# Kernel tuning notes

Hardware: AMD Instinct MI355X
Metric: run time of the kernel (lower is better)

Reference implementation:

```python
import jax, jax.numpy as jnp
import numpy as np
import math

HEIGHT = 256
THRESH = int(HEIGHT / (2 * math.sqrt(2)))  # 90, as in Spectral_Discriminator.__init__
EPS = 1e-8


def _radial_bins(h, w):
    # Static (numpy) integer radius of each pixel from the spectrum center.
    y, x = np.indices((h, w))
    cx, cy = (w - 1) / 2.0, (h - 1) / 2.0
    r = np.hypot(x - cx, y - cy)
    r_int = r.astype(np.int64).ravel()           # [h*w]
    nbins = int(r_int.max()) + 1                 # ~ h/sqrt(2) + 1 bins
    return jnp.asarray(r_int), nbins


def get_fft_feature(x):
    # x: [B, 3, H, W] -> azimuthally averaged log power spectrum [B, nbins]
    gray = 0.2989 * x[:, 0] + 0.5870 * x[:, 1] + 0.1140 * x[:, 2]   # [B,H,W]
    f = jnp.fft.fft2(gray)                                           # complex64
    mag = jnp.log(jnp.abs(f) + EPS)                                  # log magnitude
    mag = jnp.fft.fftshift(mag, axes=(-2, -1))                       # center DC
    B, h, w = mag.shape
    r_int, nbins = _radial_bins(h, w)
    flat = mag.reshape(B, -1)                                        # [B, h*w]
    # radial (azimuthal-average) binning: segment mean by integer radius
    sums = jax.vmap(lambda v: jax.ops.segment_sum(v, r_int, num_segments=nbins))(flat)
    counts = jax.ops.segment_sum(jnp.ones((h * w,), jnp.float32), r_int, num_segments=nbins)
    prof = sums / counts                                             # [B, nbins]
    # per-sample min-max normalization (NaN if max==min; masked by caller)
    mn = prof.min(axis=1, keepdims=True)
    mx = prof.max(axis=1, keepdims=True)
    return (prof - mn) / (mx - mn)


def setup_inputs() -> dict:
    key = jax.random.key(0)
    k1, k2 = jax.random.split(key)
    x = jax.random.normal(k1, (128, 3, HEIGHT, HEIGHT), dtype=jnp.float32)
    w = jax.random.normal(k2, (1, THRESH), dtype=jnp.float32) * (1.0 / math.sqrt(THRESH))
    b = jnp.zeros((1,), dtype=jnp.float32)
    return {"x": x, "w": w, "b": b}


def reference(x, w, b):
    feat = get_fft_feature(x)                          # [B, nbins]
    feat = jnp.where(jnp.isnan(feat), 0.0, feat)       # nan-masking as in forward
    feat = feat[:, -THRESH:]                           # high-frequency tail
    return feat @ w.T + b                              # [B, 1]
```

## Files before the change

### kernel.cpp

```cpp
#include <hip/hip_runtime.h>
#include <hip/hip_fp16.h>
#include <math.h>

#define NB 128
#define N 256
#define NBINS 181
#define THRESH 90
#define RS 136
#define GS 264
#define BST 137

__device__ __forceinline__ int br4(int i) {
    return ((i&1)<<3) | ((i&2)<<1) | ((i&4)>>1) | ((i&8)>>3);
}

__device__ const float TW16R[8] = { 1.f,  0.92387953f,  0.70710678f,  0.38268343f,
                                    0.f, -0.38268343f, -0.70710678f, -0.92387953f };
__device__ const float TW16I[8] = { 0.f, -0.38268343f, -0.70710678f, -0.92387953f,
                                   -1.f, -0.92387953f, -0.70710678f, -0.38268343f };
__device__ const float W256R[16] = {
    1.00000000f, 0.99969882f, 0.99879546f, 0.99729046f, 0.99518473f, 0.99247953f,
    0.98917651f, 0.98527764f, 0.98078528f, 0.97570213f, 0.97003125f, 0.96377607f,
    0.95694034f, 0.94952818f, 0.94154407f, 0.93299280f };
__device__ const float W256I[16] = {
    -0.00000000f, -0.02454123f, -0.04906767f, -0.07356456f, -0.09801714f, -0.12241068f,
    -0.14673047f, -0.17096189f, -0.19509032f, -0.21910124f, -0.24298018f, -0.26671276f,
    -0.29028468f, -0.31368174f, -0.33688985f, -0.35989504f };

__device__ __forceinline__ void fft16(float2 v[16]) {
    #pragma unroll
    for (int s = 0; s < 4; ++s) {
        const int half = 1 << s;
        #pragma unroll
        for (int gg = 0; gg < 16; gg += 2*half) {
            #pragma unroll
            for (int j = 0; j < half; ++j) {
                const float wr = TW16R[j << (3 - s)];
                const float wi = TW16I[j << (3 - s)];
                float2 a = v[gg + j], b = v[gg + j + half];
                float tr = b.x*wr - b.y*wi;
                float ti = b.x*wi + b.y*wr;
                v[gg + j]        = make_float2(a.x + tr, a.y + ti);
                v[gg + j + half] = make_float2(a.x - tr, a.y - ti);
            }
        }
    }
}

__device__ __forceinline__ void twiddle256(float2 v[16], int l) {
    const float c = W256R[l], s = W256I[l];
    float wr = c, wi = s;
    #pragma unroll
    for (int k = 1; k < 16; ++k) {
        float xr = v[k].x, xi = v[k].y;
        v[k] = make_float2(xr*wr - xi*wi, xr*wi + xi*wr);
        float nr = wr*c - wi*s;
        float ni = wr*s + wi*c;
        wr = nr; wi = ni;
    }
}

__global__ __launch_bounds__(128) void row_fft_kernel(const float* __restrict__ x,
                                                      __half2* __restrict__ F) {
    __shared__ float2 zbuf[8*GS];

    const int t = threadIdx.x;
    const int b = blockIdx.y;
    const int pbase = blockIdx.x * 8;

    const int cidx = t & 63;
    const int sub  = t >> 6;
    const float* xb = x + (size_t)b * 3 * N * N;
    #pragma unroll
    for (int i = 0; i < 4; ++i) {
        int p  = i*2 + sub;
        int r0 = (pbase + p) * 2;
        const float* p0 = xb + (size_t)r0 * N + cidx*4;
        float4 a0 = *(const float4*)(p0);
        float4 a1 = *(const float4*)(p0 + N*N);
        float4 a2 = *(const float4*)(p0 + 2*N*N);
        float4 b0 = *(const float4*)(p0 + N);
        float4 b1 = *(const float4*)(p0 + N*N + N);
        float4 b2 = *(const float4*)(p0 + 2*N*N + N);
        float gx[4], gy[4];
        #pragma unroll
        for (int j = 0; j < 4; ++j) {
            gx[j] = 0.2989f*((&a0.x)[j]) + 0.587f*((&a1.x)[j]) + 0.114f*((&a2.x)[j]);
            gy[j] = 0.2989f*((&b0.x)[j]) + 0.587f*((&b1.x)[j]) + 0.114f*((&b2.x)[j]);
        }
        *(float4*)&zbuf[p*GS + cidx*4]     = make_float4(gx[0], gy[0], gx[1], gy[1]);
        *(float4*)&zbuf[p*GS + cidx*4 + 2] = make_float4(gx[2], gy[2], gx[3], gy[3]);
    }
    __syncthreads();

    const int g = t >> 4, l = t & 15;
    float2 v[16];
    #pragma unroll
    for (int i = 0; i < 16; ++i) v[i] = zbuf[g*GS + 16*br4(i) + l];
    fft16(v);
    twiddle256(v, l);
    #pragma unroll
    for (int k = 0; k < 16; ++k) zbuf[g*GS + k*16 + ((l + k) & 15)] = v[k];
    #pragma unroll
    for (int i = 0; i < 16; ++i) v[i] = zbuf[g*GS + l*16 + ((br4(i) + l) & 15)];
    fft16(v);

    const int lane = t & 63;
    const int src  = (lane & 48) | ((16 - l) & 15);
    __half2* o0 = F + ((size_t)b * N + (size_t)(pbase + g) * 2) * RS;
    __half2* o1 = o0 + RS;
    #pragma unroll
    for (int k2 = 0; k2 < 8; ++k2) {
        float2 zm_s;
        zm_s.x = __shfl(v[15 - k2].x, src, 64);
        zm_s.y = __shfl(v[15 - k2].y, src, 64);
        float2 zm = (l == 0) ? v[(16 - k2) & 15] : zm_s;
        float2 z  = v[k2];
        int k = l + 16*k2;
        o0[k] = __floats2half2_rn(0.5f*(z.x + zm.x), 0.5f*(z.y - zm.y));
        o1[k] = __floats2half2_rn(0.5f*(z.y + zm.y), 0.5f*(zm.x - z.x));
    }
    if (l == 0) {
        float2 z = v[8];
        o0[128] = __floats2half2_rn(z.x, 0.f);
        o1[128] = __floats2half2_rn(z.y, 0.f);
    }
}

__global__ __launch_bounds__(256) void col_fft_kernel(const __half2* __restrict__ F,
                                                      __half* __restrict__ mag) {
    __shared__ float2 sbuf[16*272];
    __shared__ __half mag_lds[16*256];

    const int t = threadIdx.x;
    const int b  = blockIdx.y;
    const int cg = blockIdx.x;

    {
        const int c = t & 15, q = t >> 4;
        const int colr = cg*16 + c;
        const bool vread = (colr <= 128);
        const __half2* base = F + (size_t)b * N * RS;
        #pragma unroll
        for (int i = 0; i < 16; ++i) {
            int row = i*16 + q;
            float2 vv = vread ? __half22float2(base[(size_t)row * RS + colr])
                              : make_float2(0.f, 0.f);
            sbuf[row*17 + c] = vv;
        }
    }
    __syncthreads();

    const int g = t >> 4, l = t & 15;
    const int col = cg*16 + g;
    const bool valid = (col <= 128);
    float2 v[16];
    if (valid) {
        #pragma unroll
        for (int i = 0; i < 16; ++i) v[i] = sbuf[(16*br4(i) + l)*17 + g];
        fft16(v);
        twiddle256(v, l);
    }
    __syncthreads();

    if (valid) {
        #pragma unroll
        for (int k = 0; k < 16; ++k) sbuf[g*272 + k*17 + l] = v[k];
        #pragma unroll
        for (int i = 0; i < 16; ++i) v[i] = sbuf[g*272 + l*17 + br4(i)];
        fft16(v);
        #pragma unroll
        for (int k2 = 0; k2 < 16; ++k2) {
            float re = v[k2].x, im = v[k2].y;
            float mg = 0.5f * __logf(re*re + im*im + 1e-16f);
            int u = l + 16*k2;
            int idx = (u <= 127) ? (2*u + 1) : (2*(255 - u));
            mag_lds[g*256 + idx] = __float2half(mg);
        }
    }
    __syncthreads();

    #pragma unroll
    for (int j = 0; j < 2; ++j) {
        int flat = t + 256*j;
        int cl = flat >> 5, ch = flat & 31;
        if (cg < 8 || cl == 0) {
            int xs = (cg*16 + cl + 128) & 255;
            float4 d = *(const float4*)&mag_lds[cl*256 + ch*8];
            *(float4*)&mag[((size_t)b * 256 + xs) * 256 + ch*8] = d;
        }
    }
}

__global__ __launch_bounds__(1024) void bin_kernel(const __half* __restrict__ mag,
                                                   float* __restrict__ prof) {
    __shared__ __half2 ml[129*BST];
    const int t = threadIdx.x;
    const int q = blockIdx.x;
    const int b = blockIdx.y;
    const int lane = t & 63, wv = t >> 6;

    {
        const float4* mb4 = (const float4*)(mag + (size_t)b * 65536);
        for (int f = t; f < 4128; f += 1024) {
            int ci = f >> 5, fc = f & 31;
            int xs = (ci == 0) ? 0 : 127 + ci;
            float4 d = mb4[(size_t)xs*32 + fc];
            float* dst = (float*)&ml[ci*BST + fc*4];
            dst[0] = d.x; dst[1] = d.y; dst[2] = d.z; dst[3] = d.w;
        }
    }
    __syncthreads();

    for (int r = q + 2*wv; r < NBINS; r += 32) {
        float sum = 0.0f; int cn = 0;
        const float rr0 = (float)(r*r);
        const float rr1 = (float)((r+1)*(r+1));
        #pragma unroll
        for (int xi = 0; xi < 4; ++xi) {
            int xs = lane + 64*xi;
            float dx = (float)xs - 127.5f;
            float dx2 = dx*dx;
            float hi2 = rr1 - dx2;
            if (hi2 <= 0.0f) continue;
            float lo2 = rr0 - dx2;
            int mlo = 0;
            if (lo2 > 0.0f) mlo = (int)ceilf(sqrtf(lo2) - 0.5f);
            int mhi = (int)ceilf(sqrtf(hi2) - 0.5f);
            if (mhi > 128) mhi = 128;
            if (mlo >= mhi) continue;
            cn += 2*(mhi - mlo);
            const bool mirror = (xs >= 1) && (xs <= 127);
            int ci, jlo, jhi, aHi, bLo;
            if (!mirror) {
                ci = (xs == 0) ? 0 : xs - 127;
                jlo = mlo; jhi = mhi; aHi = mhi; bLo = mlo;
            } else {
                ci = 129 - xs;
                jlo = ((mlo > 0) ? mlo : 1) - 1;
                jhi = ((mhi < 128) ? mhi : 127) + 1;
                aHi = mhi - 1; bLo = mlo + 1;
            }
            const __half2* fp = &ml[ci*BST];
            if (mirror) {
                if (mlo == 0)   sum += __half2float(__high2half(fp[0]));
                if (mhi == 128) sum += __half2float(__low2half(fp[127]));
            }
            float s0=0.f, s1=0.f, s2=0.f, s3=0.f;
            int j = jlo;
            for (; j + 4 <= jhi; j += 4) {
                float2 a  = __half22float2(fp[j]);
                float2 bb = __half22float2(fp[j+1]);
                float2 c  = __half22float2(fp[j+2]);
                float2 d  = __half22float2(fp[j+3]);
                s0 += ((j   < aHi) ? a.x  : 0.f) + ((j   >= bLo) ? a.y  : 0.f);
                s1 += ((j+1 < aHi) ? bb.x : 0.f) + ((j+1 >= bLo) ? bb.y : 0.f);
                s2 += ((j+2 < aHi) ? c.x  : 0.f) + ((j+2 >= bLo) ? c.y  : 0.f);
                s3 += ((j+3 < aHi) ? d.x  : 0.f) + ((j+3 >= bLo) ? d.y  : 0.f);
            }
            for (; j < jhi; ++j) {
                float2 a = __half22float2(fp[j]);
                s0 += ((j < aHi) ? a.x : 0.f) + ((j >= bLo) ? a.y : 0.f);
            }
            sum += (s0 + s1) + (s2 + s3);
        }
        #pragma unroll
        for (int msk = 32; msk >= 1; msk >>= 1) {
            sum += __shfl_xor(sum, msk);
            cn  += __shfl_xor(cn,  msk);
        }
        if (lane == 0) prof[b*NBINS + r] = sum / (float)cn;
    }
}

__global__ __launch_bounds__(256) void final_kernel(const float* __restrict__ prof,
                                                    const float* __restrict__ w,
                                                    const float* __restrict__ bias,
                                                    float* __restrict__ out) {
    __shared__ float red[16];
    const int t = threadIdx.x, b = blockIdx.x;
    const int lane = t & 63, wv = t >> 6;

    float vv = (t < NBINS) ? prof[b*NBINS + t] : prof[b*NBINS];
    float mn = vv, mx = vv;
    #pragma unroll
    for (int m = 32; m >= 1; m >>= 1) {
        mn = fminf(mn, __shfl_xor(mn, m));
        mx = fmaxf(mx, __shfl_xor(mx, m));
    }
    if (lane == 0) { red[wv] = mn; red[4 + wv] = mx; }
    __syncthreads();
    if (t == 0) {
        red[8] = fminf(fminf(red[0], red[1]), fminf(red[2], red[3]));
        red[9] = fmaxf(fmaxf(red[4], red[5]), fmaxf(red[6], red[7]));
    }
    __syncthreads();
    const float mnv = red[8], mxv = red[9];

    float part = 0.0f;
    if (t < THRESH) {
        float f = (prof[b*NBINS + (NBINS - THRESH) + t] - mnv) / (mxv - mnv);
        if (f != f) f = 0.0f;
        part = f * w[t];
    }
    #pragma unroll
    for (int m = 32; m >= 1; m >>= 1) part += __shfl_xor(part, m);
    if (lane == 0) red[10 + wv] = part;
    __syncthreads();
    if (t == 0) out[b] = red[10] + red[11] + red[12] + red[13] + bias[0];
}

extern "C" void kernel_launch(void* const* d_in, const int* in_sizes, int n_in,
                              void* d_out, int out_size, void* d_ws, size_t ws_size,
                              hipStream_t stream) {
    const float* x    = (const float*)d_in[0];
    const float* w    = (const float*)d_in[1];
    const float* bias = (const float*)d_in[2];
    float* out = (float*)d_out;

    char* ws = (char*)d_ws;
    __half2* F  = (__half2*)ws;
    __half* mag = (__half*)(ws + (size_t)NB * N * RS * sizeof(__half2));
    float* prof = (float*)(ws + (size_t)NB * N * RS * sizeof(__half2)
                              + (size_t)NB * 256 * 256 * sizeof(__half));

    row_fft_kernel<<<dim3(16, NB), 128, 0, stream>>>(x, F);
    col_fft_kernel<<<dim3(9, NB), 256, 0, stream>>>(F, mag);
    bin_kernel<<<dim3(2, NB), 1024, 0, stream>>>(mag, prof);
    final_kernel<<<NB, 256, 0, stream>>>(prof, w, bias, out);
}
```

Measured before the change: 69.08 us.

## Store column-FFT LDS buffer in fp16 and split bin work by column parity

The column FFT kernel now keeps its shared transpose buffer in half2 instead of float2. This halves LDS footprint and traffic but adds an extra fp16 rounding of intermediate values after the first radix-16 stage. The binning kernel now assigns each of its two blocks per sample a disjoint set of columns (by parity) rather than a disjoint set of radii. Each block loads only half the spectrum into LDS and writes partial sums, and the final kernel adds the two partials and recomputes per-bin pixel counts analytically.

```diff
diff --git a/kernel.cpp b/kernel.cpp
--- a/kernel.cpp
+++ b/kernel.cpp
@@ -129,7 +129,7 @@
 
 __global__ __launch_bounds__(256) void col_fft_kernel(const __half2* __restrict__ F,
                                                       __half* __restrict__ mag) {
-    __shared__ float2 sbuf[16*272];
+    __shared__ __half2 sbuf[16*272];
     __shared__ __half mag_lds[16*256];
 
     const int t = threadIdx.x;
@@ -144,9 +144,8 @@
         #pragma unroll
         for (int i = 0; i < 16; ++i) {
             int row = i*16 + q;
-            float2 vv = vread ? __half22float2(base[(size_t)row * RS + colr])
-                              : make_float2(0.f, 0.f);
-            sbuf[row*17 + c] = vv;
+            sbuf[row*17 + c] = vread ? base[(size_t)row * RS + colr]
+                                     : __floats2half2_rn(0.f, 0.f);
         }
     }
     __syncthreads();
@@ -157,7 +156,7 @@
     float2 v[16];
     if (valid) {
         #pragma unroll
-        for (int i = 0; i < 16; ++i) v[i] = sbuf[(16*br4(i) + l)*17 + g];
+        for (int i = 0; i < 16; ++i) v[i] = __half22float2(sbuf[(16*br4(i) + l)*17 + g]);
         fft16(v);
         twiddle256(v, l);
     }
@@ -165,9 +164,9 @@
 
     if (valid) {
         #pragma unroll
-        for (int k = 0; k < 16; ++k) sbuf[g*272 + k*17 + l] = v[k];
-        #pragma unroll
-        for (int i = 0; i < 16; ++i) v[i] = sbuf[g*272 + l*17 + br4(i)];
+        for (int k = 0; k < 16; ++k) sbuf[g*272 + k*17 + l] = __float22half2_rn(v[k]);
+        #pragma unroll
+        for (int i = 0; i < 16; ++i) v[i] = __half22float2(sbuf[g*272 + l*17 + br4(i)]);
         fft16(v);
         #pragma unroll
         for (int k2 = 0; k2 < 16; ++k2) {
@@ -193,32 +192,34 @@
 }
 
 __global__ __launch_bounds__(1024) void bin_kernel(const __half* __restrict__ mag,
-                                                   float* __restrict__ prof) {
-    __shared__ __half2 ml[129*BST];
+                                                   float* __restrict__ prof2) {
+    __shared__ __half2 ml[65*BST];
     const int t = threadIdx.x;
     const int q = blockIdx.x;
     const int b = blockIdx.y;
     const int lane = t & 63, wv = t >> 6;
+    const int nslots = 65 - q;
 
     {
         const float4* mb4 = (const float4*)(mag + (size_t)b * 65536);
-        for (int f = t; f < 4128; f += 1024) {
-            int ci = f >> 5, fc = f & 31;
+        for (int f = t; f < nslots*32; f += 1024) {
+            int s = f >> 5, fc = f & 31;
+            int ci = q ? (2*s + 2) : ((s == 0) ? 0 : (2*s - 1));
             int xs = (ci == 0) ? 0 : 127 + ci;
             float4 d = mb4[(size_t)xs*32 + fc];
-            float* dst = (float*)&ml[ci*BST + fc*4];
+            float* dst = (float*)&ml[s*BST + fc*4];
             dst[0] = d.x; dst[1] = d.y; dst[2] = d.z; dst[3] = d.w;
         }
     }
     __syncthreads();
 
-    for (int r = q + 2*wv; r < NBINS; r += 32) {
-        float sum = 0.0f; int cn = 0;
+    for (int r = wv; r < NBINS; r += 16) {
+        float sum = 0.0f;
         const float rr0 = (float)(r*r);
         const float rr1 = (float)((r+1)*(r+1));
         #pragma unroll
-        for (int xi = 0; xi < 4; ++xi) {
-            int xs = lane + 64*xi;
+        for (int xi = 0; xi < 2; ++xi) {
+            int xs = 2*lane + q + 128*xi;
             float dx = (float)xs - 127.5f;
             float dx2 = dx*dx;
             float hi2 = rr1 - dx2;
@@ -229,7 +230,6 @@
             int mhi = (int)ceilf(sqrtf(hi2) - 0.5f);
             if (mhi > 128) mhi = 128;
             if (mlo >= mhi) continue;
-            cn += 2*(mhi - mlo);
             const bool mirror = (xs >= 1) && (xs <= 127);
             int ci, jlo, jhi, aHi, bLo;
             if (!mirror) {
@@ -241,7 +241,8 @@
                 jhi = ((mhi < 128) ? mhi : 127) + 1;
                 aHi = mhi - 1; bLo = mlo + 1;
             }
-            const __half2* fp = &ml[ci*BST];
+            const int slot = q ? ((ci - 2) >> 1) : ((ci == 0) ? 0 : ((ci + 1) >> 1));
+            const __half2* fp = &ml[slot*BST];
             if (mirror) {
                 if (mlo == 0)   sum += __half2float(__high2half(fp[0]));
                 if (mhi == 128) sum += __half2float(__low2half(fp[127]));
@@ -265,23 +266,42 @@
             sum += (s0 + s1) + (s2 + s3);
         }
         #pragma unroll
-        for (int msk = 32; msk >= 1; msk >>= 1) {
-            sum += __shfl_xor(sum, msk);
-            cn  += __shfl_xor(cn,  msk);
-        }
-        if (lane == 0) prof[b*NBINS + r] = sum / (float)cn;
-    }
-}
-
-__global__ __launch_bounds__(256) void final_kernel(const float* __restrict__ prof,
+        for (int msk = 32; msk >= 1; msk >>= 1) sum += __shfl_xor(sum, msk);
+        if (lane == 0) prof2[((size_t)q*NB + b)*NBINS + r] = sum;
+    }
+}
+
+__global__ __launch_bounds__(256) void final_kernel(const float* __restrict__ prof2,
                                                     const float* __restrict__ w,
                                                     const float* __restrict__ bias,
                                                     float* __restrict__ out) {
+    __shared__ float pr[192];
     __shared__ float red[16];
     const int t = threadIdx.x, b = blockIdx.x;
     const int lane = t & 63, wv = t >> 6;
 
-    float vv = (t < NBINS) ? prof[b*NBINS + t] : prof[b*NBINS];
+    if (t < NBINS) {
+        const float rr0 = (float)(t*t);
+        const float rr1 = (float)((t+1)*(t+1));
+        int cnt = 0;
+        for (int a = 0; a < 128; ++a) {
+            float adx = (float)a + 0.5f;
+            float d2 = adx*adx;
+            float hi2 = rr1 - d2;
+            if (hi2 <= 0.0f) continue;
+            float lo2 = rr0 - d2;
+            int mlo = 0;
+            if (lo2 > 0.0f) mlo = (int)ceilf(sqrtf(lo2) - 0.5f);
+            int mhi = (int)ceilf(sqrtf(hi2) - 0.5f);
+            if (mhi > 128) mhi = 128;
+            if (mlo < mhi) cnt += (mhi - mlo);
+        }
+        float s = prof2[(size_t)b*NBINS + t] + prof2[((size_t)NB + b)*NBINS + t];
+        pr[t] = s / (float)(4*cnt);
+    }
+    __syncthreads();
+
+    float vv = (t < NBINS) ? pr[t] : pr[0];
     float mn = vv, mx = vv;
     #pragma unroll
     for (int m = 32; m >= 1; m >>= 1) {
@@ -299,7 +319,7 @@
 
     float part = 0.0f;
     if (t < THRESH) {
-        float f = (prof[b*NBINS + (NBINS - THRESH) + t] - mnv) / (mxv - mnv);
+        float f = (pr[(NBINS - THRESH) + t] - mnv) / (mxv - mnv);
         if (f != f) f = 0.0f;
         part = f * w[t];
     }
@@ -319,13 +339,13 @@
     float* out = (float*)d_out;
 
     char* ws = (char*)d_ws;
-    __half2* F  = (__half2*)ws;
-    __half* mag = (__half*)(ws + (size_t)NB * N * RS * sizeof(__half2));
-    float* prof = (float*)(ws + (size_t)NB * N * RS * sizeof(__half2)
-                              + (size_t)NB * 256 * 256 * sizeof(__half));
+    __half2* F   = (__half2*)ws;
+    __half* mag  = (__half*)(ws + (size_t)NB * N * RS * sizeof(__half2));
+    float* prof2 = (float*)(ws + (size_t)NB * N * RS * sizeof(__half2)
+                               + (size_t)NB * 256 * 256 * sizeof(__half));
 
     row_fft_kernel<<<dim3(16, NB), 128, 0, stream>>>(x, F);
     col_fft_kernel<<<dim3(9, NB), 256, 0, stream>>>(F, mag);
-    bin_kernel<<<dim3(2, NB), 1024, 0, stream>>>(mag, prof);
-    final_kernel<<<NB, 256, 0, stream>>>(prof, w, bias, out);
-}
+    bin_kernel<<<dim3(2, NB), 1024, 0, stream>>>(mag, prof2);
+    final_kernel<<<NB, 256, 0, stream>>>(prof2, w, bias, out);
+}
```

After: 86.10 us. 1.25x slower.
